# Performance work log

Hardware: AMD Instinct MI355X
Metric: run time of the kernel (lower is better)

## Reference

```python
import jax, jax.numpy as jnp
import numpy as np

N_HEADS = 32
N_KV_HEADS = 8
HEAD_DIM = 128  # hidden 4096 / 32
NEG_INF = -1e9


def _apply_rope(x, cos, sin):
    # x: [B, S, H, D]; cos/sin: [S, D//2] -> complex multiply on (even, odd) pairs
    B, S, H, D = x.shape
    xr = x.reshape(B, S, H, D // 2, 2)
    a, b = xr[..., 0], xr[..., 1]
    c = cos[None, :, None, :]
    s = sin[None, :, None, :]
    out = jnp.stack([a * c - b * s, a * s + b * c], axis=-1)
    return out.reshape(B, S, H, D)


def setup_inputs() -> dict:
    key = jax.random.key(0)
    ks = jax.random.split(key, 8)
    B, S, HID = 1, 2048, 4096
    hidden_states = jax.random.normal(ks[0], (B, S, HID), dtype=jnp.float32)
    # causal additive mask [1,1,S,S]
    causal = jnp.tril(jnp.ones((S, S), dtype=bool))
    attention_mask = jnp.where(causal, 0.0, NEG_INF).astype(jnp.float32)[None, None]
    # true rotary frequencies (theta=500000 as in llama3)
    half = HEAD_DIM // 2
    inv_freq = 1.0 / (500000.0 ** (np.arange(0, half, dtype=np.float32) / half))
    angles = np.arange(S, dtype=np.float32)[:, None] * inv_freq[None, :]
    freqs_cos = jnp.asarray(np.cos(angles), dtype=jnp.float32)
    freqs_sin = jnp.asarray(np.sin(angles), dtype=jnp.float32)
    sc = 0.02
    wq = jax.random.normal(ks[1], (HID, HID), dtype=jnp.float32) * sc
    wk = jax.random.normal(ks[2], (N_KV_HEADS * HEAD_DIM, HID), dtype=jnp.float32) * sc
    wv = jax.random.normal(ks[3], (N_KV_HEADS * HEAD_DIM, HID), dtype=jnp.float32) * sc
    wo = jax.random.normal(ks[4], (HID, HID), dtype=jnp.float32) * sc
    return {"hidden_states": hidden_states, "attention_mask": attention_mask,
            "freqs_cos": freqs_cos, "freqs_sin": freqs_sin,
            "wq": wq, "wk": wk, "wv": wv, "wo": wo}


def reference(hidden_states, attention_mask, freqs_cos, freqs_sin, wq, wk, wv, wo):
    B, S, HID = hidden_states.shape
    n_rep = N_HEADS // N_KV_HEADS
    # projections (torch Linear: x @ W.T)
    q = (hidden_states @ wq.T).reshape(B, S, N_HEADS, HEAD_DIM)
    k = (hidden_states @ wk.T).reshape(B, S, N_KV_HEADS, HEAD_DIM)
    v = (hidden_states @ wv.T).reshape(B, S, N_KV_HEADS, HEAD_DIM)
    # rotary on q (full cos/sin) and k
    q = _apply_rope(q, freqs_cos, freqs_sin)
    k = _apply_rope(k, freqs_cos, freqs_sin)
    # [B, H, S, D]
    q = q.transpose(0, 2, 1, 3)
    k = k.transpose(0, 2, 1, 3)
    v = v.transpose(0, 2, 1, 3)
    # GQA: repeat_interleave kv heads
    k = jnp.repeat(k, n_rep, axis=1)
    v = jnp.repeat(v, n_rep, axis=1)
    scores = jnp.einsum("bhqd,bhkd->bhqk", q, k) / jnp.sqrt(jnp.float32(HEAD_DIM))
    scores = scores + attention_mask
    probs = jax.nn.softmax(scores.astype(jnp.float32), axis=-1)
    attn = jnp.einsum("bhqk,bhkd->bhqd", probs, v)
    attn = attn.transpose(0, 2, 1, 3).reshape(B, S, N_HEADS * HEAD_DIM)
    return attn @ wo.T
```

## Files before the change

### kernel.cpp

```cpp
#include <hip/hip_runtime.h>
#include <hip/hip_bf16.h>
#include <math.h>

#define SEQ 2048
#define HID 4096
#define NH 32
#define NKV 8
#define HD 128
#define KVG (NH / NKV)
#define NQKV 6144

typedef __bf16 bf16x8 __attribute__((ext_vector_type(8)));
typedef float  f32x4  __attribute__((ext_vector_type(4)));

__device__ __forceinline__ unsigned short f2bf(float f) {
  union { float f; unsigned int u; } v; v.f = f;
  unsigned int r = v.u + 0x7FFFu + ((v.u >> 16) & 1u);
  return (unsigned short)(r >> 16);
}
__device__ __forceinline__ float bf2f(unsigned short h) {
  union { unsigned int u; float f; } v; v.u = ((unsigned int)h) << 16;
  return v.f;
}

__device__ __forceinline__ void glds16(const unsigned short* g, unsigned short* l) {
  __builtin_amdgcn_global_load_lds(
      (const __attribute__((address_space(1))) void*)g,
      (__attribute__((address_space(3))) void*)l, 16, 0, 0);
}

#define MFMA_BF16 __builtin_amdgcn_mfma_f32_16x16x32_bf16

__global__ __launch_bounds__(256) void cvt_all(
    const float* __restrict__ H, const float* __restrict__ wq,
    const float* __restrict__ wk, const float* __restrict__ wv,
    const float* __restrict__ wo, unsigned short* __restrict__ ws)
{
  const long G1 = 1l << 20;
  const long M1 = 1l << 20;
  long g = (long)blockIdx.x * 256 + threadIdx.x;
  const float* src; unsigned short* dst; long rel;
  if      (g < 2 * G1) { src = H;  dst = ws;           rel = g;          }
  else if (g < 6 * G1) { src = wq; dst = ws + 8 * M1;  rel = g - 2 * G1; }
  else if (g < 7 * G1) { src = wk; dst = ws + 24 * M1; rel = g - 6 * G1; }
  else if (g < 8 * G1) { src = wv; dst = ws + 28 * M1; rel = g - 7 * G1; }
  else                 { src = wo; dst = ws + 32 * M1; rel = g - 8 * G1; }
  float4 v = ((const float4*)src)[rel];
  ushort4 o;
  o.x = f2bf(v.x); o.y = f2bf(v.y); o.z = f2bf(v.z); o.w = f2bf(v.w);
  ((ushort4*)dst)[rel] = o;
}

__global__ __launch_bounds__(512, 2) void gemm_qkv(
    const unsigned short* __restrict__ A,
    const unsigned short* __restrict__ B,
    unsigned short* __restrict__ C,
    int M, int N, int K)
{
  __shared__ unsigned short As[2][256 * 64];
  __shared__ unsigned short Bs[2][192 * 64];
  const int t = threadIdx.x;
  const int lane = t & 63, wid = t >> 6;
  const int quad = lane >> 4, l16 = lane & 15;
  const int wm = wid >> 2, wn = wid & 3;
  const int m0 = blockIdx.y * 256, n0 = blockIdx.x * 192;
  const int U = K >> 7;
  const int lrow8 = lane >> 3;
  const int gch = (lane & 7) ^ lrow8;

  const unsigned short* gA[4];
  const unsigned short* gB[3];
  #pragma unroll
  for (int ua = 0; ua < 4; ua++)
    gA[ua] = A + (size_t)(m0 + ua * 64 + wid * 8 + lrow8) * K + gch * 8;
  #pragma unroll
  for (int ub = 0; ub < 3; ub++)
    gB[ub] = B + (size_t)(n0 + ub * 64 + wid * 8 + lrow8) * K + gch * 8;

  auto stA = [&](int ua, int buf, int kt) {
    glds16(gA[ua] + (size_t)kt * 64, &As[buf][(ua * 64 + wid * 8) * 64]);
  };
  auto stB = [&](int ub, int buf, int kt) {
    glds16(gB[ub] + (size_t)kt * 64, &Bs[buf][(ub * 64 + wid * 8) * 64]);
  };
  auto ldA = [&](int buf, int mt, int ks) -> bf16x8 {
    int row = wm * 128 + mt * 16 + l16;
    int cp = (ks * 4 + quad) ^ (l16 & 7);
    return *(const bf16x8*)(&As[buf][row * 64 + cp * 8]);
  };
  auto ldB = [&](int buf, int nt, int ks) -> bf16x8 {
    int row = wn * 48 + nt * 16 + l16;
    int cp = (ks * 4 + quad) ^ (l16 & 7);
    return *(const bf16x8*)(&Bs[buf][row * 64 + cp * 8]);
  };

  const f32x4 fzero = {0.f, 0.f, 0.f, 0.f};
  f32x4 acc[8][3];
  #pragma unroll
  for (int i = 0; i < 8; i++)
    #pragma unroll
    for (int j = 0; j < 3; j++) acc[i][j] = fzero;

  #pragma unroll
  for (int ua = 0; ua < 4; ua++) stA(ua, 0, 0);
  #pragma unroll
  for (int ub = 0; ub < 3; ub++) stB(ub, 0, 0);
  stB(0, 1, 1); stB(1, 1, 1); stB(2, 1, 1);
  stA(0, 1, 1); stA(2, 1, 1); stA(1, 1, 1);
  asm volatile("s_waitcnt vmcnt(6)" ::: "memory");
  __builtin_amdgcn_s_barrier();

  bf16x8 fa[4][2], fb[3][2];

  for (int u = 0; u < U; u++) {
    const bool last = (u == U - 1);
    const int k1 = 2 * u + 1, k2 = 2 * u + 2, k3 = 2 * u + 3;

    #pragma unroll
    for (int mt = 0; mt < 4; mt++)
      #pragma unroll
      for (int ks = 0; ks < 2; ks++) fa[mt][ks] = ldA(0, mt, ks);
    #pragma unroll
    for (int nt = 0; nt < 3; nt++)
      #pragma unroll
      for (int ks = 0; ks < 2; ks++) fb[nt][ks] = ldB(0, nt, ks);
    stA(3, 1, k1);
    __builtin_amdgcn_s_barrier();
    asm volatile("s_waitcnt lgkmcnt(0)" ::: "memory");
    __builtin_amdgcn_s_setprio(1);
    #pragma unroll
    for (int mt = 0; mt < 4; mt++)
      #pragma unroll
      for (int nt = 0; nt < 2; nt++)
        #pragma unroll
        for (int ks = 0; ks < 2; ks++)
          acc[mt][nt] = MFMA_BF16(fa[mt][ks], fb[nt][ks], acc[mt][nt], 0, 0, 0);
    __builtin_amdgcn_s_setprio(0);
    __builtin_amdgcn_s_barrier();

    if (!last) { stB(0, 0, k2); stB(1, 0, k2); }
    __builtin_amdgcn_s_barrier();
    __builtin_amdgcn_s_setprio(1);
    #pragma unroll
    for (int mt = 0; mt < 4; mt++)
      #pragma unroll
      for (int ks = 0; ks < 2; ks++)
        acc[mt][2] = MFMA_BF16(fa[mt][ks], fb[2][ks], acc[mt][2], 0, 0, 0);
    __builtin_amdgcn_s_setprio(0);
    __builtin_amdgcn_s_barrier();

    #pragma unroll
    for (int mt = 0; mt < 4; mt++)
      #pragma unroll
      for (int ks = 0; ks < 2; ks++) fa[mt][ks] = ldA(0, 4 + mt, ks);
    if (!last) { stB(2, 0, k2); stA(0, 0, k2); }
    __builtin_amdgcn_s_barrier();
    asm volatile("s_waitcnt lgkmcnt(0)" ::: "memory");
    __builtin_amdgcn_s_setprio(1);
    #pragma unroll
    for (int mt = 0; mt < 4; mt++)
      #pragma unroll
      for (int nt = 0; nt < 2; nt++)
        #pragma unroll
        for (int ks = 0; ks < 2; ks++)
          acc[4 + mt][nt] = MFMA_BF16(fa[mt][ks], fb[nt][ks], acc[4 + mt][nt], 0, 0, 0);
    __builtin_amdgcn_s_setprio(0);
    __builtin_amdgcn_s_barrier();

    if (!last) { stA(2, 0, k2); stA(1, 0, k2); }
    __builtin_amdgcn_s_barrier();
    __builtin_amdgcn_s_setprio(1);
    #pragma unroll
    for (int mt = 0; mt < 4; mt++)
      #pragma unroll
      for (int ks = 0; ks < 2; ks++)
        acc[4 + mt][2] = MFMA_BF16(fa[mt][ks], fb[2][ks], acc[4 + mt][2], 0, 0, 0);
    __builtin_amdgcn_s_setprio(0);
    if (!last) asm volatile("s_waitcnt vmcnt(6)" ::: "memory");
    else       asm volatile("s_waitcnt vmcnt(0)" ::: "memory");
    __builtin_amdgcn_s_barrier();

    #pragma unroll
    for (int mt = 0; mt < 4; mt++)
      #pragma unroll
      for (int ks = 0; ks < 2; ks++) fa[mt][ks] = ldA(1, mt, ks);
    #pragma unroll
    for (int nt = 0; nt < 3; nt++)
      #pragma unroll
      for (int ks = 0; ks < 2; ks++) fb[nt][ks] = ldB(1, nt, ks);
    if (!last) stA(3, 0, k2);
    __builtin_amdgcn_s_barrier();
    asm volatile("s_waitcnt lgkmcnt(0)" ::: "memory");
    __builtin_amdgcn_s_setprio(1);
    #pragma unroll
    for (int mt = 0; mt < 4; mt++)
      #pragma unroll
      for (int nt = 0; nt < 2; nt++)
        #pragma unroll
        for (int ks = 0; ks < 2; ks++)
          acc[mt][nt] = MFMA_BF16(fa[mt][ks], fb[nt][ks], acc[mt][nt], 0, 0, 0);
    __builtin_amdgcn_s_setprio(0);
    __builtin_amdgcn_s_barrier();

    if (!last) { stB(0, 1, k3); stB(1, 1, k3); }
    __builtin_amdgcn_s_barrier();
    __builtin_amdgcn_s_setprio(1);
    #pragma unroll
    for (int mt = 0; mt < 4; mt++)
      #pragma unroll
      for (int ks = 0; ks < 2; ks++)
        acc[mt][2] = MFMA_BF16(fa[mt][ks], fb[2][ks], acc[mt][2], 0, 0, 0);
    __builtin_amdgcn_s_setprio(0);
    __builtin_amdgcn_s_barrier();

    #pragma unroll
    for (int mt = 0; mt < 4; mt++)
      #pragma unroll
      for (int ks = 0; ks < 2; ks++) fa[mt][ks] = ldA(1, 4 + mt, ks);
    if (!last) { stB(2, 1, k3); stA(0, 1, k3); }
    __builtin_amdgcn_s_barrier();
    asm volatile("s_waitcnt lgkmcnt(0)" ::: "memory");
    __builtin_amdgcn_s_setprio(1);
    #pragma unroll
    for (int mt = 0; mt < 4; mt++)
      #pragma unroll
      for (int nt = 0; nt < 2; nt++)
        #pragma unroll
        for (int ks = 0; ks < 2; ks++)
          acc[4 + mt][nt] = MFMA_BF16(fa[mt][ks], fb[nt][ks], acc[4 + mt][nt], 0, 0, 0);
    __builtin_amdgcn_s_setprio(0);
    __builtin_amdgcn_s_barrier();

    if (!last) { stA(2, 1, k3); stA(1, 1, k3); }
    __builtin_amdgcn_s_barrier();
    __builtin_amdgcn_s_setprio(1);
    #pragma unroll
    for (int mt = 0; mt < 4; mt++)
      #pragma unroll
      for (int ks = 0; ks < 2; ks++)
        acc[4 + mt][2] = MFMA_BF16(fa[mt][ks], fb[2][ks], acc[4 + mt][2], 0, 0, 0);
    __builtin_amdgcn_s_setprio(0);
    if (!last) asm volatile("s_waitcnt vmcnt(6)" ::: "memory");
    __builtin_amdgcn_s_barrier();
  }

  #pragma unroll
  for (int mt = 0; mt < 8; mt++)
    #pragma unroll
    for (int nt = 0; nt < 3; nt++)
      #pragma unroll
      for (int r = 0; r < 4; r++) {
        int row = m0 + wm * 128 + mt * 16 + quad * 4 + r;
        int col = n0 + wn * 48 + nt * 16 + l16;
        C[(size_t)row * N + col] = f2bf(acc[mt][nt][r]);
      }
}

template<bool F32OUT>
__global__ __launch_bounds__(256) void gemm_nt(
    const unsigned short* __restrict__ A,
    const unsigned short* __restrict__ B,
    void* __restrict__ Cv,
    int M, int N, int K)
{
  __shared__ unsigned short As[128 * 64];
  __shared__ unsigned short Bs[128 * 64];
  const int t = threadIdx.x;
  const int lane = t & 63, wid = t >> 6;
  const int quad = lane >> 4, l16 = lane & 15;
  const int wm = (wid & 1) * 64, wn = (wid >> 1) * 64;
  const int m0 = blockIdx.y * 128, n0 = blockIdx.x * 128;

  int srow[4], sgch[4];
  const unsigned short* ga[4];
  const unsigned short* gb[4];
  unsigned short* la[4];
  unsigned short* lb[4];
  #pragma unroll
  for (int j = 0; j < 4; j++) {
    int pj = (wid * 4 + j) * 64 + lane;
    srow[j] = pj >> 3;
    sgch[j] = (pj & 7) ^ (srow[j] & 7);
    ga[j] = A + (size_t)(m0 + srow[j]) * K + sgch[j] * 8;
    gb[j] = B + (size_t)(n0 + srow[j]) * K + sgch[j] * 8;
    la[j] = &As[(wid * 4 + j) * 512];
    lb[j] = &Bs[(wid * 4 + j) * 512];
  }

  const f32x4 fzero = {0.f, 0.f, 0.f, 0.f};
  f32x4 acc[4][4];
  #pragma unroll
  for (int i = 0; i < 4; i++)
    #pragma unroll
    for (int j = 0; j < 4; j++) acc[i][j] = fzero;

  for (int k0 = 0; k0 < K; k0 += 64) {
    __syncthreads();
    #pragma unroll
    for (int j = 0; j < 4; j++) {
      glds16(ga[j], la[j]);
      glds16(gb[j], lb[j]);
      ga[j] += 64; gb[j] += 64;
    }
    __syncthreads();

    #pragma unroll
    for (int ks = 0; ks < 2; ks++) {
      bf16x8 af[4], bfr[4];
      #pragma unroll
      for (int mt = 0; mt < 4; mt++) {
        int row = wm + mt * 16 + l16;
        int cp = (ks * 4 + quad) ^ (l16 & 7);
        af[mt] = *(const bf16x8*)(&As[(row * 8 + cp) * 8]);
      }
      #pragma unroll
      for (int nt = 0; nt < 4; nt++) {
        int row = wn + nt * 16 + l16;
        int cp = (ks * 4 + quad) ^ (l16 & 7);
        bfr[nt] = *(const bf16x8*)(&Bs[(row * 8 + cp) * 8]);
      }
      #pragma unroll
      for (int mt = 0; mt < 4; mt++)
        #pragma unroll
        for (int nt = 0; nt < 4; nt++)
          acc[mt][nt] = MFMA_BF16(af[mt], bfr[nt], acc[mt][nt], 0, 0, 0);
    }
  }

  #pragma unroll
  for (int mt = 0; mt < 4; mt++)
    #pragma unroll
    for (int nt = 0; nt < 4; nt++)
      #pragma unroll
      for (int r = 0; r < 4; r++) {
        int row = m0 + wm + mt * 16 + quad * 4 + r;
        int col = n0 + wn + nt * 16 + l16;
        float v = acc[mt][nt][r];
        if (F32OUT) ((float*)Cv)[(size_t)row * N + col] = v;
        else        ((unsigned short*)Cv)[(size_t)row * N + col] = f2bf(v);
      }
}

__global__ __launch_bounds__(256) void rope_vtrans(
    const unsigned short* __restrict__ QKVr,
    const float* __restrict__ cosT,
    const float* __restrict__ sinT,
    unsigned short* __restrict__ Qh,
    unsigned short* __restrict__ Kh,
    unsigned short* __restrict__ Vtg)
{
  __shared__ unsigned short T[64 * 66];
  int hh = blockIdx.y;
  int bx = blockIdx.x;
  int t = threadIdx.x;
  if (hh < NH + NKV) {
    int sub = t >> 6, d2 = t & 63;
    int s = bx * 4 + sub;
    float c = cosT[s * 64 + d2], sn = sinT[s * 64 + d2];
    if (hh < NH) {
      const unsigned short* src = QKVr + (size_t)s * NQKV + hh * HD;
      unsigned short* dst = Qh + ((size_t)hh * SEQ + s) * HD;
      float a = bf2f(src[2 * d2]), b = bf2f(src[2 * d2 + 1]);
      dst[2 * d2]     = f2bf(a * c - b * sn);
      dst[2 * d2 + 1] = f2bf(a * sn + b * c);
    } else {
      int h = hh - NH;
      const unsigned short* src = QKVr + (size_t)s * NQKV + HID + h * HD;
      unsigned short* dst = Kh + ((size_t)h * SEQ + s) * HD;
      float a = bf2f(src[2 * d2]), b = bf2f(src[2 * d2 + 1]);
      dst[2 * d2]     = f2bf(a * c - b * sn);
      dst[2 * d2 + 1] = f2bf(a * sn + b * c);
    }
  } else {
    int idx = bx >> 5;
    int kvh = idx >> 1, d0 = (idx & 1) * 64;
    int s0 = (bx & 31) * 64;
    int si = t >> 2, dchunk = t & 3;
    const unsigned short* src = QKVr + (size_t)(s0 + si) * NQKV + HID + NKV * HD + kvh * HD + d0 + dchunk * 16;
    uint4 a = *(const uint4*)src;
    uint4 b = *(const uint4*)(src + 8);
    unsigned int va[8] = {a.x, a.y, a.z, a.w, b.x, b.y, b.z, b.w};
    #pragma unroll
    for (int j = 0; j < 8; j++)
      *(unsigned int*)(&T[si * 66 + dchunk * 16 + j * 2]) = va[j];
    __syncthreads();
    int di = t >> 2, schunk = t & 3;
    unsigned short px[16];
    #pragma unroll
    for (int j = 0; j < 16; j++) px[j] = T[(schunk * 16 + j) * 66 + di];
    unsigned short* dst = Vtg + ((size_t)kvh * HD + d0 + di) * SEQ + s0 + schunk * 16;
    *(uint4*)dst = *(uint4*)px;
    *(uint4*)(dst + 8) = *(uint4*)(px + 8);
  }
}

__global__ __launch_bounds__(256) void flash_kernel(
    const unsigned short* __restrict__ Qh,
    const unsigned short* __restrict__ Kh,
    const unsigned short* __restrict__ Vtg,
    unsigned short* __restrict__ Obf)
{
  __shared__ unsigned short Ks[64 * 128];
  __shared__ unsigned short Vs[128 * 64];
  __shared__ unsigned short Ps[4][16 * 72];

  const int h = blockIdx.y;
  const int pairp = blockIdx.x;
  const int kvh = h / KVG;
  const int t = threadIdx.x;
  const int lane = t & 63, w = t >> 6;
  const int quad = lane >> 4, l16 = lane & 15;
  const float scale = 0.08838834764831845f;
  const float SHIFT = 8.0f;

  bf16x8 ones;
  #pragma unroll
  for (int j = 0; j < 8; j++) ones[j] = (__bf16)1.0f;

  int krow[4], kgch[4], vrow[4], vgch[4];
  unsigned short* lk[4];
  unsigned short* lv[4];
  #pragma unroll
  for (int j = 0; j < 4; j++) {
    int pj = (w * 4 + j) * 64 + lane;
    krow[j] = pj >> 4; kgch[j] = (pj & 15) ^ (krow[j] & 15);
    vrow[j] = pj >> 3; vgch[j] = (pj & 7) ^ (vrow[j] & 7);
    lk[j] = &Ks[(w * 4 + j) * 512];
    lv[j] = &Vs[(w * 4 + j) * 512];
  }

  unsigned short* Pw = Ps[w];
  const f32x4 fzero = {0.f, 0.f, 0.f, 0.f};

  #pragma unroll
  for (int pass = 0; pass < 2; pass++) {
    const int qt = pass ? (31 - pairp) : pairp;
    const int q0 = qt * 64;
    const int q = q0 + w * 16 + l16;

    bf16x8 aq[4];
    const unsigned short* Qp = Qh + ((size_t)h * SEQ + q0 + w * 16 + l16) * HD;
    #pragma unroll
    for (int ks = 0; ks < 4; ks++) aq[ks] = *(const bf16x8*)(Qp + ks * 32 + quad * 8);

    f32x4 o[8];
    #pragma unroll
    for (int dt = 0; dt < 8; dt++) o[dt] = fzero;
    f32x4 lacc = fzero;

    const unsigned short* gk[4];
    const unsigned short* gv[4];
    #pragma unroll
    for (int j = 0; j < 4; j++) {
      gk[j] = Kh + ((size_t)kvh * SEQ + krow[j]) * HD + kgch[j] * 8;
      gv[j] = Vtg + ((size_t)kvh * HD + vrow[j]) * SEQ + vgch[j] * 8;
    }

    for (int kv0 = 0; kv0 <= q0; kv0 += 64) {
      __syncthreads();
      #pragma unroll
      for (int j = 0; j < 4; j++) {
        glds16(gk[j], lk[j]);
        glds16(gv[j], lv[j]);
        gk[j] += 64 * HD;
        gv[j] += 64;
      }
      __syncthreads();

      f32x4 sc[4];
      #pragma unroll
      for (int kvt = 0; kvt < 4; kvt++) sc[kvt] = fzero;
      #pragma unroll
      for (int ks = 0; ks < 4; ks++)
        #pragma unroll
        for (int kvt = 0; kvt < 4; kvt++) {
          int row = kvt * 16 + l16;
          int cp = (ks * 4 + quad) ^ l16;
          bf16x8 bk = *(const bf16x8*)(&Ks[(row * 16 + cp) * 8]);
          sc[kvt] = MFMA_BF16(bk, aq[ks], sc[kvt], 0, 0, 0);
        }

      #pragma unroll
      for (int kvt = 0; kvt < 4; kvt++) {
        unsigned short ph[4];
        #pragma unroll
        for (int r = 0; r < 4; r++) {
          int kv = kv0 + kvt * 16 + quad * 4 + r;
          float p = (kv > q) ? 0.f : __expf(fmaf(sc[kvt][r], scale, -SHIFT));
          ph[r] = f2bf(p);
        }
        *(uint2*)(&Pw[l16 * 72 + kvt * 16 + quad * 4]) = *(const uint2*)ph;
      }

      #pragma unroll
      for (int ks2 = 0; ks2 < 2; ks2++) {
        bf16x8 ap = *(const bf16x8*)(&Pw[l16 * 72 + ks2 * 32 + quad * 8]);
        lacc = MFMA_BF16(ap, ones, lacc, 0, 0, 0);
        #pragma unroll
        for (int dt = 0; dt < 8; dt++) {
          int row = dt * 16 + l16;
          int cp = (ks2 * 4 + quad) ^ (l16 & 7);
          bf16x8 bv = *(const bf16x8*)(&Vs[(row * 8 + cp) * 8]);
          o[dt] = MFMA_BF16(ap, bv, o[dt], 0, 0, 0);
        }
      }
    }

    #pragma unroll
    for (int dt = 0; dt < 8; dt++)
      #pragma unroll
      for (int r = 0; r < 4; r++) {
        int qq = q0 + w * 16 + quad * 4 + r;
        int d = dt * 16 + l16;
        Obf[(size_t)qq * HID + h * HD + d] = f2bf(o[dt][r] / lacc[r]);
      }
  }
}

extern "C" void kernel_launch(void* const* d_in, const int* in_sizes, int n_in,
                              void* d_out, int out_size, void* d_ws, size_t ws_size,
                              hipStream_t stream) {
  const float* H    = (const float*)d_in[0];
  const float* cosT = (const float*)d_in[2];
  const float* sinT = (const float*)d_in[3];
  const float* wq   = (const float*)d_in[4];
  const float* wk   = (const float*)d_in[5];
  const float* wv   = (const float*)d_in[6];
  const float* wo   = (const float*)d_in[7];

  unsigned short* ws = (unsigned short*)d_ws;
  const size_t M1 = 1u << 20;
  unsigned short* Hb   = ws;
  unsigned short* Wqkv = ws + (size_t)8  * M1;
  unsigned short* Wob  = ws + (size_t)32 * M1;
  unsigned short* QKVr = ws + (size_t)48 * M1;
  unsigned short* Qh   = ws + (size_t)8  * M1;
  unsigned short* Kh   = ws + (size_t)16 * M1;
  unsigned short* Vtg  = ws + (size_t)18 * M1;
  unsigned short* attn = ws;

  cvt_all<<<49152, 256, 0, stream>>>(H, wq, wk, wv, wo, ws);

  gemm_qkv<<<dim3(32, 8), 512, 0, stream>>>(Hb, Wqkv, QKVr, SEQ, NQKV, HID);

  rope_vtrans<<<dim3(512, NH + NKV + 1), 256, 0, stream>>>(QKVr, cosT, sinT, Qh, Kh, Vtg);

  flash_kernel<<<dim3(16, NH), 256, 0, stream>>>(Qh, Kh, Vtg, attn);

  gemm_nt<true><<<dim3(32, 16), 256, 0, stream>>>(attn, Wob, d_out, SEQ, HID, HID);
}
```

Measured before the change: 487.5 us.

## Software-pipeline LDS fragment loads one phase ahead of MFMA blocks in QKV GEMM

Restructures the GEMM main loop so that the LDS fragment reads for the next group of M-tiles are issued before the MFMAs of the current group. The explicit lgkmcnt(0) waits are removed, so LDS read latency can overlap with matrix math instead of stalling each phase. The cost is more fragment registers held at once (separate even and odd buffers), which raises register pressure and could hurt occupancy or cause spills. The barrier and prefetch ordering also become more intricate.

```diff
diff --git a/kernel.cpp b/kernel.cpp
--- a/kernel.cpp
+++ b/kernel.cpp
@@ -101,146 +101,178 @@
     #pragma unroll
     for (int j = 0; j < 3; j++) acc[i][j] = fzero;
 
+  bf16x8 faE[4][2][2], faO[4][2][2], fbE[3][2], fbO[3][2];
+
   #pragma unroll
   for (int ua = 0; ua < 4; ua++) stA(ua, 0, 0);
   #pragma unroll
   for (int ub = 0; ub < 3; ub++) stB(ub, 0, 0);
   stB(0, 1, 1); stB(1, 1, 1); stB(2, 1, 1);
-  stA(0, 1, 1); stA(2, 1, 1); stA(1, 1, 1);
+  stA(0, 1, 1); stA(1, 1, 1); stA(2, 1, 1);
   asm volatile("s_waitcnt vmcnt(6)" ::: "memory");
   __builtin_amdgcn_s_barrier();
-
-  bf16x8 fa[4][2], fb[3][2];
+  #pragma unroll
+  for (int nt = 0; nt < 3; nt++)
+    #pragma unroll
+    for (int ks = 0; ks < 2; ks++) fbE[nt][ks] = ldB(0, nt, ks);
+  #pragma unroll
+  for (int i = 0; i < 2; i++)
+    #pragma unroll
+    for (int ks = 0; ks < 2; ks++) faE[0][i][ks] = ldA(0, i, ks);
 
   for (int u = 0; u < U; u++) {
-    const bool last = (u == U - 1);
-    const int k1 = 2 * u + 1, k2 = 2 * u + 2, k3 = 2 * u + 3;
-
-    #pragma unroll
-    for (int mt = 0; mt < 4; mt++)
-      #pragma unroll
-      for (int ks = 0; ks < 2; ks++) fa[mt][ks] = ldA(0, mt, ks);
+    const bool lastu = (u == U - 1);
+    const int ke = 2 * u, ko = 2 * u + 1;
+
+    stA(3, 1, ke + 1);
+    #pragma unroll
+    for (int i = 0; i < 2; i++)
+      #pragma unroll
+      for (int ks = 0; ks < 2; ks++) faE[1][i][ks] = ldA(0, 2 + i, ks);
+    __builtin_amdgcn_s_barrier();
+    __builtin_amdgcn_s_setprio(1);
+    #pragma unroll
+    for (int i = 0; i < 2; i++)
+      #pragma unroll
+      for (int nt = 0; nt < 3; nt++)
+        #pragma unroll
+        for (int ks = 0; ks < 2; ks++)
+          acc[i][nt] = MFMA_BF16(faE[0][i][ks], fbE[nt][ks], acc[i][nt], 0, 0, 0);
+    __builtin_amdgcn_s_setprio(0);
+    __builtin_amdgcn_s_barrier();
+
+    if (!lastu) { stB(0, 0, ke + 2); stB(1, 0, ke + 2); }
+    #pragma unroll
+    for (int i = 0; i < 2; i++)
+      #pragma unroll
+      for (int ks = 0; ks < 2; ks++) faE[2][i][ks] = ldA(0, 4 + i, ks);
+    __builtin_amdgcn_s_barrier();
+    __builtin_amdgcn_s_setprio(1);
+    #pragma unroll
+    for (int i = 0; i < 2; i++)
+      #pragma unroll
+      for (int nt = 0; nt < 3; nt++)
+        #pragma unroll
+        for (int ks = 0; ks < 2; ks++)
+          acc[2 + i][nt] = MFMA_BF16(faE[1][i][ks], fbE[nt][ks], acc[2 + i][nt], 0, 0, 0);
+    __builtin_amdgcn_s_setprio(0);
+    __builtin_amdgcn_s_barrier();
+
+    if (!lastu) { stB(2, 0, ke + 2); stA(0, 0, ke + 2); }
+    #pragma unroll
+    for (int i = 0; i < 2; i++)
+      #pragma unroll
+      for (int ks = 0; ks < 2; ks++) faE[3][i][ks] = ldA(0, 6 + i, ks);
+    __builtin_amdgcn_s_barrier();
+    __builtin_amdgcn_s_setprio(1);
+    #pragma unroll
+    for (int i = 0; i < 2; i++)
+      #pragma unroll
+      for (int nt = 0; nt < 3; nt++)
+        #pragma unroll
+        for (int ks = 0; ks < 2; ks++)
+          acc[4 + i][nt] = MFMA_BF16(faE[2][i][ks], fbE[nt][ks], acc[4 + i][nt], 0, 0, 0);
+    __builtin_amdgcn_s_setprio(0);
+    __builtin_amdgcn_s_barrier();
+
+    if (!lastu) { stA(1, 0, ke + 2); stA(2, 0, ke + 2); }
+    if (!lastu) asm volatile("s_waitcnt vmcnt(6)" ::: "memory");
+    else        asm volatile("s_waitcnt vmcnt(0)" ::: "memory");
+    __builtin_amdgcn_s_barrier();
     #pragma unroll
     for (int nt = 0; nt < 3; nt++)
       #pragma unroll
-      for (int ks = 0; ks < 2; ks++) fb[nt][ks] = ldB(0, nt, ks);
-    stA(3, 1, k1);
-    __builtin_amdgcn_s_barrier();
-    asm volatile("s_waitcnt lgkmcnt(0)" ::: "memory");
-    __builtin_amdgcn_s_setprio(1);
-    #pragma unroll
-    for (int mt = 0; mt < 4; mt++)
-      #pragma unroll
-      for (int nt = 0; nt < 2; nt++)
-        #pragma unroll
-        for (int ks = 0; ks < 2; ks++)
-          acc[mt][nt] = MFMA_BF16(fa[mt][ks], fb[nt][ks], acc[mt][nt], 0, 0, 0);
-    __builtin_amdgcn_s_setprio(0);
-    __builtin_amdgcn_s_barrier();
-
-    if (!last) { stB(0, 0, k2); stB(1, 0, k2); }
-    __builtin_amdgcn_s_barrier();
-    __builtin_amdgcn_s_setprio(1);
-    #pragma unroll
-    for (int mt = 0; mt < 4; mt++)
-      #pragma unroll
-      for (int ks = 0; ks < 2; ks++)
-        acc[mt][2] = MFMA_BF16(fa[mt][ks], fb[2][ks], acc[mt][2], 0, 0, 0);
-    __builtin_amdgcn_s_setprio(0);
-    __builtin_amdgcn_s_barrier();
-
-    #pragma unroll
-    for (int mt = 0; mt < 4; mt++)
-      #pragma unroll
-      for (int ks = 0; ks < 2; ks++) fa[mt][ks] = ldA(0, 4 + mt, ks);
-    if (!last) { stB(2, 0, k2); stA(0, 0, k2); }
-    __builtin_amdgcn_s_barrier();
-    asm volatile("s_waitcnt lgkmcnt(0)" ::: "memory");
-    __builtin_amdgcn_s_setprio(1);
-    #pragma unroll
-    for (int mt = 0; mt < 4; mt++)
-      #pragma unroll
-      for (int nt = 0; nt < 2; nt++)
-        #pragma unroll
-        for (int ks = 0; ks < 2; ks++)
-          acc[4 + mt][nt] = MFMA_BF16(fa[mt][ks], fb[nt][ks], acc[4 + mt][nt], 0, 0, 0);
-    __builtin_amdgcn_s_setprio(0);
-    __builtin_amdgcn_s_barrier();
-
-    if (!last) { stA(2, 0, k2); stA(1, 0, k2); }
-    __builtin_amdgcn_s_barrier();
-    __builtin_amdgcn_s_setprio(1);
-    #pragma unroll
-    for (int mt = 0; mt < 4; mt++)
-      #pragma unroll
-      for (int ks = 0; ks < 2; ks++)
-        acc[4 + mt][2] = MFMA_BF16(fa[mt][ks], fb[2][ks], acc[4 + mt][2], 0, 0, 0);
-    __builtin_amdgcn_s_setprio(0);
-    if (!last) asm volatile("s_waitcnt vmcnt(6)" ::: "memory");
-    else       asm volatile("s_waitcnt vmcnt(0)" ::: "memory");
-    __builtin_amdgcn_s_barrier();
-
-    #pragma unroll
-    for (int mt = 0; mt < 4; mt++)
-      #pragma unroll
-      for (int ks = 0; ks < 2; ks++) fa[mt][ks] = ldA(1, mt, ks);
-    #pragma unroll
-    for (int nt = 0; nt < 3; nt++)
-      #pragma unroll
-      for (int ks = 0; ks < 2; ks++) fb[nt][ks] = ldB(1, nt, ks);
-    if (!last) stA(3, 0, k2);
-    __builtin_amdgcn_s_barrier();
-    asm volatile("s_waitcnt lgkmcnt(0)" ::: "memory");
-    __builtin_amdgcn_s_setprio(1);
-    #pragma unroll
-    for (int mt = 0; mt < 4; mt++)
-      #pragma unroll
-      for (int nt = 0; nt < 2; nt++)
-        #pragma unroll
-        for (int ks = 0; ks < 2; ks++)
-          acc[mt][nt] = MFMA_BF16(fa[mt][ks], fb[nt][ks], acc[mt][nt], 0, 0, 0);
-    __builtin_amdgcn_s_setprio(0);
-    __builtin_amdgcn_s_barrier();
-
-    if (!last) { stB(0, 1, k3); stB(1, 1, k3); }
-    __builtin_amdgcn_s_barrier();
-    __builtin_amdgcn_s_setprio(1);
-    #pragma unroll
-    for (int mt = 0; mt < 4; mt++)
-      #pragma unroll
-      for (int ks = 0; ks < 2; ks++)
-        acc[mt][2] = MFMA_BF16(fa[mt][ks], fb[2][ks], acc[mt][2], 0, 0, 0);
-    __builtin_amdgcn_s_setprio(0);
-    __builtin_amdgcn_s_barrier();
-
-    #pragma unroll
-    for (int mt = 0; mt < 4; mt++)
-      #pragma unroll
-      for (int ks = 0; ks < 2; ks++) fa[mt][ks] = ldA(1, 4 + mt, ks);
-    if (!last) { stB(2, 1, k3); stA(0, 1, k3); }
-    __builtin_amdgcn_s_barrier();
-    asm volatile("s_waitcnt lgkmcnt(0)" ::: "memory");
-    __builtin_amdgcn_s_setprio(1);
-    #pragma unroll
-    for (int mt = 0; mt < 4; mt++)
-      #pragma unroll
-      for (int nt = 0; nt < 2; nt++)
-        #pragma unroll
-        for (int ks = 0; ks < 2; ks++)
-          acc[4 + mt][nt] = MFMA_BF16(fa[mt][ks], fb[nt][ks], acc[4 + mt][nt], 0, 0, 0);
-    __builtin_amdgcn_s_setprio(0);
-    __builtin_amdgcn_s_barrier();
-
-    if (!last) { stA(2, 1, k3); stA(1, 1, k3); }
-    __builtin_amdgcn_s_barrier();
-    __builtin_amdgcn_s_setprio(1);
-    #pragma unroll
-    for (int mt = 0; mt < 4; mt++)
-      #pragma unroll
-      for (int ks = 0; ks < 2; ks++)
-        acc[4 + mt][2] = MFMA_BF16(fa[mt][ks], fb[2][ks], acc[4 + mt][2], 0, 0, 0);
-    __builtin_amdgcn_s_setprio(0);
-    if (!last) asm volatile("s_waitcnt vmcnt(6)" ::: "memory");
+      for (int ks = 0; ks < 2; ks++) fbO[nt][ks] = ldB(1, nt, ks);
+    #pragma unroll
+    for (int i = 0; i < 2; i++)
+      #pragma unroll
+      for (int ks = 0; ks < 2; ks++) faO[0][i][ks] = ldA(1, i, ks);
+    __builtin_amdgcn_s_setprio(1);
+    #pragma unroll
+    for (int i = 0; i < 2; i++)
+      #pragma unroll
+      for (int nt = 0; nt < 3; nt++)
+        #pragma unroll
+        for (int ks = 0; ks < 2; ks++)
+          acc[6 + i][nt] = MFMA_BF16(faE[3][i][ks], fbE[nt][ks], acc[6 + i][nt], 0, 0, 0);
+    __builtin_amdgcn_s_setprio(0);
+    __builtin_amdgcn_s_barrier();
+
+    if (!lastu) stA(3, 0, ko + 1);
+    #pragma unroll
+    for (int i = 0; i < 2; i++)
+      #pragma unroll
+      for (int ks = 0; ks < 2; ks++) faO[1][i][ks] = ldA(1, 2 + i, ks);
+    __builtin_amdgcn_s_barrier();
+    __builtin_amdgcn_s_setprio(1);
+    #pragma unroll
+    for (int i = 0; i < 2; i++)
+      #pragma unroll
+      for (int nt = 0; nt < 3; nt++)
+        #pragma unroll
+        for (int ks = 0; ks < 2; ks++)
+          acc[i][nt] = MFMA_BF16(faO[0][i][ks], fbO[nt][ks], acc[i][nt], 0, 0, 0);
+    __builtin_amdgcn_s_setprio(0);
+    __builtin_amdgcn_s_barrier();
+
+    if (!lastu) { stB(0, 1, ko + 2); stB(1, 1, ko + 2); }
+    #pragma unroll
+    for (int i = 0; i < 2; i++)
+      #pragma unroll
+      for (int ks = 0; ks < 2; ks++) faO[2][i][ks] = ldA(1, 4 + i, ks);
+    __builtin_amdgcn_s_barrier();
+    __builtin_amdgcn_s_setprio(1);
+    #pragma unroll
+    for (int i = 0; i < 2; i++)
+      #pragma unroll
+      for (int nt = 0; nt < 3; nt++)
+        #pragma unroll
+        for (int ks = 0; ks < 2; ks++)
+          acc[2 + i][nt] = MFMA_BF16(faO[1][i][ks], fbO[nt][ks], acc[2 + i][nt], 0, 0, 0);
+    __builtin_amdgcn_s_setprio(0);
+    __builtin_amdgcn_s_barrier();
+
+    if (!lastu) { stB(2, 1, ko + 2); stA(0, 1, ko + 2); }
+    #pragma unroll
+    for (int i = 0; i < 2; i++)
+      #pragma unroll
+      for (int ks = 0; ks < 2; ks++) faO[3][i][ks] = ldA(1, 6 + i, ks);
+    __builtin_amdgcn_s_barrier();
+    __builtin_amdgcn_s_setprio(1);
+    #pragma unroll
+    for (int i = 0; i < 2; i++)
+      #pragma unroll
+      for (int nt = 0; nt < 3; nt++)
+        #pragma unroll
+        for (int ks = 0; ks < 2; ks++)
+          acc[4 + i][nt] = MFMA_BF16(faO[2][i][ks], fbO[nt][ks], acc[4 + i][nt], 0, 0, 0);
+    __builtin_amdgcn_s_setprio(0);
+    __builtin_amdgcn_s_barrier();
+
+    if (!lastu) { stA(1, 1, ko + 2); stA(2, 1, ko + 2); }
+    if (!lastu) {
+      asm volatile("s_waitcnt vmcnt(6)" ::: "memory");
+      __builtin_amdgcn_s_barrier();
+      #pragma unroll
+      for (int nt = 0; nt < 3; nt++)
+        #pragma unroll
+        for (int ks = 0; ks < 2; ks++) fbE[nt][ks] = ldB(0, nt, ks);
+      #pragma unroll
+      for (int i = 0; i < 2; i++)
+        #pragma unroll
+        for (int ks = 0; ks < 2; ks++) faE[0][i][ks] = ldA(0, i, ks);
+    } else {
+      __builtin_amdgcn_s_barrier();
+    }
+    __builtin_amdgcn_s_setprio(1);
+    #pragma unroll
+    for (int i = 0; i < 2; i++)
+      #pragma unroll
+      for (int nt = 0; nt < 3; nt++)
+        #pragma unroll
+        for (int ks = 0; ks < 2; ks++)
+          acc[6 + i][nt] = MFMA_BF16(faO[3][i][ks], fbO[nt][ks], acc[6 + i][nt], 0, 0, 0);
+    __builtin_amdgcn_s_setprio(0);
     __builtin_amdgcn_s_barrier();
   }
 
```

New measurement: 528.6 us. 1.08x slower.
